# Kernel optimization log

Hardware: AMD Instinct MI355X
Metric: run time of the kernel (lower is better)

Reference implementation:

```python
import jax, jax.numpy as jnp
import numpy as np

CH = 256  # channels

def setup_inputs() -> dict:
    key = jax.random.key(0)
    ks = jax.random.split(key, 9)
    B, H, W = 8, 64, 64
    c8, c2 = CH // 8, CH // 2
    s = lambda fan_in: 1.0 / np.sqrt(fan_in)
    return {
        "x": jax.random.normal(ks[0], (B, H, W, CH), dtype=jnp.float32),
        "Wq": jax.random.normal(ks[1], (CH, c8), dtype=jnp.float32) * s(CH),
        "bq": jnp.zeros((c8,), dtype=jnp.float32),
        "Wk": jax.random.normal(ks[2], (CH, c8), dtype=jnp.float32) * s(CH),
        "bk": jnp.zeros((c8,), dtype=jnp.float32),
        "Wv": jax.random.normal(ks[3], (CH, c2), dtype=jnp.float32) * s(CH),
        "bv": jnp.zeros((c2,), dtype=jnp.float32),
        "Wo": jax.random.normal(ks[4], (c2, CH), dtype=jnp.float32) * s(c2),
        "bo": jnp.zeros((CH,), dtype=jnp.float32),
    }

def reference(x, Wq, bq, Wk, bk, Wv, bv, Wo, bo):
    B, H, W, C = x.shape
    # 1x1 convs are per-pixel matmuls over the channel dim
    q = x @ Wq + bq                      # [B,H,W,C/8]
    k = x @ Wk + bk                      # [B,H,W,C/8]
    v = x @ Wv + bv                      # [B,H,W,C/2]
    N = H * W
    qf = q.reshape(B, N, -1)
    kf = k.reshape(B, N, -1)
    vf = v.reshape(B, N, -1)
    # full self-attention over flattened spatial positions (no scaling, per source)
    scores = jnp.einsum('bnd,bmd->bnm', qf, kf)   # [B,N,N]
    attn = jax.nn.softmax(scores, axis=-1)
    out = jnp.einsum('bnm,bmd->bnd', attn, vf)    # [B,N,C/2]
    out = out.reshape(B, H, W, -1)
    return out @ Wo + bo + x
```

## Files before the change

### kernel.cpp

```cpp
#include <hip/hip_runtime.h>

typedef __attribute__((ext_vector_type(8))) short short8;
typedef __attribute__((ext_vector_type(8))) _Float16 half8;
typedef __attribute__((ext_vector_type(2))) float f32x2;
typedef __attribute__((ext_vector_type(4))) float f32x4;
typedef __attribute__((ext_vector_type(16))) float f32x16;

__device__ __forceinline__ unsigned short f2bf(float f) {
  unsigned int u = __float_as_uint(f);
  u += 0x7fffu + ((u >> 16) & 1u);
  return (unsigned short)(u >> 16);
}
__device__ __forceinline__ float bf2f(unsigned short h) {
  return __uint_as_float(((unsigned int)h) << 16);
}
__device__ __forceinline__ unsigned int cvtpk(float a, float b) {
  unsigned int r;
  asm("v_cvt_pk_bf16_f32 %0, %1, %2" : "=v"(r) : "v"(a), "v"(b));
  return r;
}
__device__ __forceinline__ unsigned short f2h(float f) {
  unsigned int r;
  asm("v_cvt_f16_f32 %0, %1" : "=v"(r) : "v"(f));
  return (unsigned short)r;
}
__device__ __forceinline__ float lo16f(unsigned int u) { return __uint_as_float(u << 16); }
__device__ __forceinline__ float hi16f(unsigned int u) { return __uint_as_float(u & 0xffff0000u); }
__device__ __forceinline__ short8 ld8(const unsigned short* p) {
  return *(const short8*)p;
}
__device__ __forceinline__ half8 ld8h(const unsigned short* p) {
  return *(const half8*)p;
}
__device__ __forceinline__ int swap23(int x) {
  return (x & 0x13) | ((x & 4) << 1) | ((x & 8) >> 1);
}
#define MFMA(a, b, c) __builtin_amdgcn_mfma_f32_16x16x32_bf16((a), (b), (c), 0, 0, 0)
#define MFMA32(a, b, c) __builtin_amdgcn_mfma_f32_32x32x16_bf16((a), (b), (c), 0, 0, 0)
#define MFMA32H(a, b, c) __builtin_amdgcn_mfma_f32_32x32x16_f16((a), (b), (c), 0, 0, 0)
#define LOG2E 1.4426950408889634f

typedef const __attribute__((address_space(1))) unsigned int* gas_u32p;
typedef __attribute__((address_space(3))) unsigned int* las_u32p;

__global__ void prep_weights(const float* __restrict__ Wq, const float* __restrict__ Wk,
                             const float* __restrict__ Wv, const float* __restrict__ Wo,
                             unsigned short* __restrict__ Wth, unsigned short* __restrict__ Wtl,
                             unsigned short* __restrict__ WoT) {
  int idx = blockIdx.x * 256 + threadIdx.x;
  if (idx < 192 * 256) {
    int o = idx >> 8, c = idx & 255;
    float w = (o < 32) ? Wq[c * 32 + o] : (o < 64) ? Wk[c * 32 + (o - 32)] : Wv[c * 128 + (o - 64)];
    unsigned short h = f2bf(w);
    Wth[idx] = h;
    Wtl[idx] = f2bf(w - bf2f(h));
  } else if (idx < 192 * 256 + 256 * 128) {
    int j = idx - 192 * 256;
    int c = j >> 7, d = j & 127;
    WoT[j] = f2bf(Wo[d * 256 + c]);
  }
}

__global__ __launch_bounds__(256) void proj_qkv(
    const float* __restrict__ x,
    const unsigned short* __restrict__ Wth, const unsigned short* __restrict__ Wtl,
    const float* __restrict__ bq, const float* __restrict__ bk, const float* __restrict__ bv,
    unsigned short* __restrict__ qh, unsigned short* __restrict__ KVF) {
  __shared__ unsigned short xsh[32][264];
  __shared__ unsigned short xsl[32][264];
  const int pix0 = blockIdx.x * 32;
  const int b = pix0 >> 12;
  const int nloc0 = pix0 & 4095;
  const int tid = threadIdx.x;

#pragma unroll
  for (int i = 0; i < 8; ++i) {
    int chunk = i * 256 + tid;
    int row = chunk >> 6;
    int c4 = (chunk & 63) * 4;
    float4 v = *(const float4*)(x + (size_t)(pix0 + row) * 256 + c4);
    unsigned int h01 = cvtpk(v.x, v.y), h23 = cvtpk(v.z, v.w);
    unsigned int l01 = cvtpk(v.x - lo16f(h01), v.y - hi16f(h01));
    unsigned int l23 = cvtpk(v.z - lo16f(h23), v.w - hi16f(h23));
    uint2 hp, lp;
    hp.x = h01; hp.y = h23;
    lp.x = l01; lp.y = l23;
    *(uint2*)&xsh[row][c4] = hp;
    *(uint2*)&xsl[row][c4] = lp;
  }
  __syncthreads();

  const int wave = tid >> 6, lane = tid & 63, l = lane & 15, qd = lane >> 4;
#pragma unroll
  for (int si = 0; si < 3; ++si) {
    const int sub = wave + si * 4;
    const int outc0 = sub * 16;
    if (si == 0) {
      const int outc = outc0 + l;
      const float bias = (outc < 32) ? bq[outc] : bk[outc - 32];
      f32x4 acc[2];
      acc[0] = (f32x4){bias, bias, bias, bias};
      acc[1] = (f32x4){bias, bias, bias, bias};
#pragma unroll
      for (int kc = 0; kc < 8; ++kc) {
        short8 whf = ld8(Wth + (size_t)(outc0 + l) * 256 + kc * 32 + qd * 8);
        short8 wlf = ld8(Wtl + (size_t)(outc0 + l) * 256 + kc * 32 + qd * 8);
#pragma unroll
        for (int m = 0; m < 2; ++m) {
          short8 xhf = ld8(&xsh[m * 16 + l][kc * 32 + qd * 8]);
          short8 xlf = ld8(&xsl[m * 16 + l][kc * 32 + qd * 8]);
          acc[m] = MFMA(xlf, whf, acc[m]);
          acc[m] = MFMA(xhf, wlf, acc[m]);
          acc[m] = MFMA(xhf, whf, acc[m]);
        }
      }
      if (outc < 32) {
#pragma unroll
        for (int m = 0; m < 2; ++m)
#pragma unroll
          for (int r = 0; r < 4; ++r) {
            const size_t pixel = (size_t)pix0 + m * 16 + 4 * qd + r;
            qh[pixel * 32 + outc] = f2h(acc[m][r] * LOG2E);
          }
      } else {
        const int kd = outc - 32;
        const int step = kd >> 4, hh = (kd >> 3) & 1, e = kd & 7;
#pragma unroll
        for (int m = 0; m < 2; ++m)
#pragma unroll
          for (int r = 0; r < 4; ++r) {
            const int nl = nloc0 + m * 16 + 4 * qd + r;
            const int nt = nl >> 6, j = nl & 63, kt = j >> 5;
            const int lpos = swap23(j & 31);
            const size_t koff = (size_t)(b * 64 + nt) * 10240 +
                                (kt * 2 + step) * 512 + (hh * 32 + lpos) * 8 + e;
            KVF[koff] = f2h(acc[m][r]);
          }
      }
    } else {
      const int dv0 = outc0 - 64;
      const float b0 = bv[dv0 + 4 * qd + 0], b1 = bv[dv0 + 4 * qd + 1];
      const float b2 = bv[dv0 + 4 * qd + 2], b3 = bv[dv0 + 4 * qd + 3];
      f32x4 acc[2];
      acc[0] = (f32x4){b0, b1, b2, b3};
      acc[1] = (f32x4){b0, b1, b2, b3};
#pragma unroll
      for (int kc = 0; kc < 8; ++kc) {
        short8 whf = ld8(Wth + (size_t)(outc0 + l) * 256 + kc * 32 + qd * 8);
#pragma unroll
        for (int m = 0; m < 2; ++m) {
          short8 xhf = ld8(&xsh[m * 16 + l][kc * 32 + qd * 8]);
          acc[m] = MFMA(whf, xhf, acc[m]);
        }
      }
#pragma unroll
      for (int m = 0; m < 2; ++m)
#pragma unroll
        for (int r = 0; r < 4; ++r) {
          const int dv = dv0 + 4 * qd + r;
          const int dt = dv >> 5, lam = dv & 31;
          const int nl = nloc0 + m * 16 + l;
          const int nt = nl >> 6, j = nl & 63;
          const int ks = j >> 4, hh = (j >> 3) & 1, e = j & 7;
          const size_t voff = (size_t)(b * 64 + nt) * 10240 + 2048 +
                              (dt * 4 + ks) * 512 + (hh * 32 + lam) * 8 + e;
          KVF[voff] = (unsigned short)cvtpk(acc[m][r], acc[m][r]);
        }
    }
  }
}

__device__ __forceinline__ void stage_kv(const unsigned short* __restrict__ src,
                                         unsigned short* dst, int wave, int lane) {
#pragma unroll
  for (int i = 0; i < 5; ++i) {
    const int c = wave * 5 + i;
    __builtin_amdgcn_global_load_lds(
        (gas_u32p)(const void*)(src + c * 512 + lane * 8),
        (las_u32p)(void*)(dst + c * 512), 16, 0, 0);
  }
}

__global__ __launch_bounds__(256, 2) void flash_attn(
    const unsigned short* __restrict__ qh,
    const unsigned short* __restrict__ KVF, unsigned short* __restrict__ opart,
    float* __restrict__ lstat) {
  __shared__ unsigned short kv[2][10240];
  const int b = blockIdx.x & 7;
  const int r7 = blockIdx.x >> 3;
  const int tile = r7 & 15;
  const int split = r7 >> 4;
  const int wave = threadIdx.x >> 6;
  const int lane = threadIdx.x & 63;
  const int lam = lane & 31;
  const int h = lane >> 5;
  const int m0 = tile * 256 + wave * 64;
  const int nt0 = split * 16;

  const unsigned short* qh_b = qh + (size_t)b * 4096 * 32;
  const unsigned short* kv_b = KVF + (size_t)b * 64 * 10240;

  half8 qf[2][2];
#pragma unroll
  for (int t = 0; t < 2; ++t)
#pragma unroll
    for (int step = 0; step < 2; ++step)
      qf[t][step] = ld8h(qh_b + (size_t)(m0 + t * 32 + lam) * 32 + step * 16 + h * 8);

  f32x16 acc0[4], acc1[4];
#pragma unroll
  for (int dt = 0; dt < 4; ++dt)
#pragma unroll
    for (int e = 0; e < 16; ++e) { acc0[dt][e] = 0.f; acc1[dt][e] = 0.f; }
  f32x2 lr0 = (f32x2){0.f, 0.f}, lr1 = (f32x2){0.f, 0.f};

  stage_kv(kv_b + (size_t)nt0 * 10240, &kv[0][0], wave, lane);
  __syncthreads();

  int cur = 0;
#pragma unroll 1
  for (int it = 0; it < 16; ++it) {
    if (it < 15)
      stage_kv(kv_b + (size_t)(nt0 + it + 1) * 10240, &kv[cur ^ 1][0], wave, lane);

    const unsigned short* cb = &kv[cur][0];

    half8 k0a = ld8h(cb + 0 * 512 + lane * 8);
    half8 k0b = ld8h(cb + 1 * 512 + lane * 8);
    f32x16 z0, z1;
#pragma unroll
    for (int e = 0; e < 16; ++e) { z0[e] = 0.f; z1[e] = 0.f; }
    __builtin_amdgcn_s_setprio(1);
    z0 = MFMA32H(k0a, qf[0][0], z0);
    z0 = MFMA32H(k0b, qf[0][1], z0);
    z1 = MFMA32H(k0a, qf[1][0], z1);
    z1 = MFMA32H(k0b, qf[1][1], z1);
    __builtin_amdgcn_s_setprio(0);
    unsigned int ppA0[8], ppA1[8];
#pragma unroll
    for (int g = 0; g < 8; ++g) {
      float a0 = __builtin_amdgcn_exp2f(z0[2 * g]);
      float a1 = __builtin_amdgcn_exp2f(z0[2 * g + 1]);
      lr0 += (f32x2){a0, a1};
      ppA0[g] = cvtpk(a0, a1);
      float c0 = __builtin_amdgcn_exp2f(z1[2 * g]);
      float c1 = __builtin_amdgcn_exp2f(z1[2 * g + 1]);
      lr1 += (f32x2){c0, c1};
      ppA1[g] = cvtpk(c0, c1);
    }

    half8 k1a = ld8h(cb + 2 * 512 + lane * 8);
    half8 k1b = ld8h(cb + 3 * 512 + lane * 8);
    f32x16 w0, w1;
#pragma unroll
    for (int e = 0; e < 16; ++e) { w0[e] = 0.f; w1[e] = 0.f; }
    __builtin_amdgcn_s_setprio(1);
    w0 = MFMA32H(k1a, qf[0][0], w0);
    w0 = MFMA32H(k1b, qf[0][1], w0);
    w1 = MFMA32H(k1a, qf[1][0], w1);
    w1 = MFMA32H(k1b, qf[1][1], w1);
#pragma unroll
    for (int kss = 0; kss < 2; ++kss) {
      union { unsigned int u[4]; short8 v; } pf0, pf1;
#pragma unroll
      for (int j = 0; j < 4; ++j) { pf0.u[j] = ppA0[4 * kss + j]; pf1.u[j] = ppA1[4 * kss + j]; }
#pragma unroll
      for (int dt = 0; dt < 4; ++dt) {
        short8 vfrag = *(const short8*)(cb + 2048 + (dt * 4 + kss) * 512 + lane * 8);
        acc0[dt] = MFMA32(vfrag, pf0.v, acc0[dt]);
        acc1[dt] = MFMA32(vfrag, pf1.v, acc1[dt]);
      }
    }
    __builtin_amdgcn_s_setprio(0);
    unsigned int ppB0[8], ppB1[8];
#pragma unroll
    for (int g = 0; g < 8; ++g) {
      float a0 = __builtin_amdgcn_exp2f(w0[2 * g]);
      float a1 = __builtin_amdgcn_exp2f(w0[2 * g + 1]);
      lr0 += (f32x2){a0, a1};
      ppB0[g] = cvtpk(a0, a1);
      float c0 = __builtin_amdgcn_exp2f(w1[2 * g]);
      float c1 = __builtin_amdgcn_exp2f(w1[2 * g + 1]);
      lr1 += (f32x2){c0, c1};
      ppB1[g] = cvtpk(c0, c1);
    }
    __builtin_amdgcn_s_setprio(1);
#pragma unroll
    for (int kss = 0; kss < 2; ++kss) {
      union { unsigned int u[4]; short8 v; } pf0, pf1;
#pragma unroll
      for (int j = 0; j < 4; ++j) { pf0.u[j] = ppB0[4 * kss + j]; pf1.u[j] = ppB1[4 * kss + j]; }
#pragma unroll
      for (int dt = 0; dt < 4; ++dt) {
        short8 vfrag = *(const short8*)(cb + 2048 + (dt * 4 + 2 + kss) * 512 + lane * 8);
        acc0[dt] = MFMA32(vfrag, pf0.v, acc0[dt]);
        acc1[dt] = MFMA32(vfrag, pf1.v, acc1[dt]);
      }
    }
    __builtin_amdgcn_s_setprio(0);

    __syncthreads();
    cur ^= 1;
  }

  {
    const float lrun = lr0.x + lr0.y;
    const float ltot = lrun + __shfl_xor(lrun, 32);
    const int grow = b * 4096 + m0 + lam;
    if (h == 0) lstat[split * 32768 + grow] = ltot;
    const size_t obase = ((size_t)split * 32768 + grow) * 128;
#pragma unroll
    for (int dt = 0; dt < 4; ++dt)
#pragma unroll
      for (int g = 0; g < 8; ++g) {
        int r = 2 * g;
        int dv = dt * 32 + (r & 3) + 8 * (r >> 2) + 4 * h;
        *(unsigned int*)(opart + obase + dv) = cvtpk(acc0[dt][r], acc0[dt][r + 1]);
      }
  }
  {
    const float lrun = lr1.x + lr1.y;
    const float ltot = lrun + __shfl_xor(lrun, 32);
    const int grow = b * 4096 + m0 + 32 + lam;
    if (h == 0) lstat[split * 32768 + grow] = ltot;
    const size_t obase = ((size_t)split * 32768 + grow) * 128;
#pragma unroll
    for (int dt = 0; dt < 4; ++dt)
#pragma unroll
      for (int g = 0; g < 8; ++g) {
        int r = 2 * g;
        int dv = dt * 32 + (r & 3) + 8 * (r >> 2) + 4 * h;
        *(unsigned int*)(opart + obase + dv) = cvtpk(acc1[dt][r], acc1[dt][r + 1]);
      }
  }
}

__global__ __launch_bounds__(256) void combine_splits(
    const unsigned short* __restrict__ opart, const float* __restrict__ lstat,
    unsigned short* __restrict__ ao) {
  const int tid = threadIdx.x;
  const int row = blockIdx.x * 16 + (tid >> 4);
  const int col = (tid & 15) * 8;
  float den = lstat[row] + lstat[32768 + row] + lstat[65536 + row] + lstat[98304 + row];
  float inv = 1.f / den;
  float o[8] = {0.f, 0.f, 0.f, 0.f, 0.f, 0.f, 0.f, 0.f};
#pragma unroll
  for (int s = 0; s < 4; ++s) {
    uint4 v = *(const uint4*)(opart + ((size_t)s * 32768 + row) * 128 + col);
    unsigned int uu[4] = {v.x, v.y, v.z, v.w};
#pragma unroll
    for (int j = 0; j < 4; ++j) {
      o[2 * j]     += bf2f((unsigned short)(uu[j] & 0xffff));
      o[2 * j + 1] += bf2f((unsigned short)(uu[j] >> 16));
    }
  }
  uint4 outv;
  outv.x = cvtpk(o[0] * inv, o[1] * inv);
  outv.y = cvtpk(o[2] * inv, o[3] * inv);
  outv.z = cvtpk(o[4] * inv, o[5] * inv);
  outv.w = cvtpk(o[6] * inv, o[7] * inv);
  *(uint4*)(ao + (size_t)row * 128 + col) = outv;
}

__global__ __launch_bounds__(256) void out_proj(
    const unsigned short* __restrict__ ao, const unsigned short* __restrict__ WoT,
    const float* __restrict__ bo, const float* __restrict__ x, float* __restrict__ out) {
  const int pix0 = blockIdx.x * 64;
  const int wave = threadIdx.x >> 6, lane = threadIdx.x & 63, l = lane & 15, qd = lane >> 4;
  const int base = pix0 + wave * 16;
  short8 af[4];
#pragma unroll
  for (int kc = 0; kc < 4; ++kc)
    af[kc] = ld8(ao + (size_t)(base + l) * 128 + kc * 32 + qd * 8);
#pragma unroll
  for (int sub = 0; sub < 16; ++sub) {
    const int c0 = sub * 16 + 4 * qd;
    float4 bb = *(const float4*)(bo + c0);
    f32x4 acc = (f32x4){bb.x, bb.y, bb.z, bb.w};
#pragma unroll
    for (int kc = 0; kc < 4; ++kc) {
      short8 wf = ld8(WoT + (size_t)(sub * 16 + l) * 128 + kc * 32 + qd * 8);
      acc = MFMA(wf, af[kc], acc);
    }
    float4 xv = *(const float4*)(x + (size_t)(base + l) * 256 + c0);
    float4 res;
    res.x = acc[0] + xv.x;
    res.y = acc[1] + xv.y;
    res.z = acc[2] + xv.z;
    res.w = acc[3] + xv.w;
    *(float4*)(out + (size_t)(base + l) * 256 + c0) = res;
  }
}

extern "C" void kernel_launch(void* const* d_in, const int* in_sizes, int n_in,
                              void* d_out, int out_size, void* d_ws, size_t ws_size,
                              hipStream_t stream) {
  const float* x  = (const float*)d_in[0];
  const float* Wq = (const float*)d_in[1];
  const float* bq = (const float*)d_in[2];
  const float* Wk = (const float*)d_in[3];
  const float* bk = (const float*)d_in[4];
  const float* Wv = (const float*)d_in[5];
  const float* bv = (const float*)d_in[6];
  const float* Wo = (const float*)d_in[7];
  const float* bo = (const float*)d_in[8];

  char* ws = (char*)d_ws;
  unsigned short* qh  = (unsigned short*)(ws + 0);
  unsigned short* KVF = (unsigned short*)(ws + 2097152);
  unsigned short* ao  = (unsigned short*)(ws + 12582912);
  unsigned short* Wth = (unsigned short*)(ws + 20971520);
  unsigned short* Wtl = (unsigned short*)(ws + 21069824);
  unsigned short* WoT = (unsigned short*)(ws + 21168128);
  float*          lst = (float*)(ws + 21233664);
  unsigned short* opart = (unsigned short*)d_out;

  prep_weights<<<320, 256, 0, stream>>>(Wq, Wk, Wv, Wo, Wth, Wtl, WoT);
  proj_qkv<<<1024, 256, 0, stream>>>(x, Wth, Wtl, bq, bk, bv, qh, KVF);
  flash_attn<<<512, 256, 0, stream>>>(qh, KVF, opart, lst);
  combine_splits<<<2048, 256, 0, stream>>>(opart, lst, ao);
  out_proj<<<512, 256, 0, stream>>>(ao, WoT, bo, x, (float*)d_out);
}
```

Measured before the change: 191.4 us.

## Halve rows per wave and use three KV splits with more blocks

The flash attention kernel now gives each wave 32 query rows instead of 64 and splits the key range into 3 uneven chunks instead of 4. This triples the block count relative to tiles and allows 3 blocks per CU via launch bounds. The combine kernel now sums 3 partials. The goal is to improve occupancy and load balance and to cut the combine traffic. The trade-off is less K/V reuse per LDS stage, so each query row needs twice the staging traffic.

```diff
diff --git a/kernel.cpp b/kernel.cpp
--- a/kernel.cpp
+++ b/kernel.cpp
@@ -181,120 +181,105 @@
   }
 }
 
-__global__ __launch_bounds__(256, 2) void flash_attn(
+__global__ __launch_bounds__(256, 3) void flash_attn(
     const unsigned short* __restrict__ qh,
     const unsigned short* __restrict__ KVF, unsigned short* __restrict__ opart,
     float* __restrict__ lstat) {
   __shared__ unsigned short kv[2][10240];
   const int b = blockIdx.x & 7;
   const int r7 = blockIdx.x >> 3;
-  const int tile = r7 & 15;
-  const int split = r7 >> 4;
+  const int tile = r7 & 31;
+  const int split = r7 >> 5;
   const int wave = threadIdx.x >> 6;
   const int lane = threadIdx.x & 63;
   const int lam = lane & 31;
   const int h = lane >> 5;
-  const int m0 = tile * 256 + wave * 64;
-  const int nt0 = split * 16;
+  const int m0 = tile * 128 + wave * 32;
+  const int nt_begin = (split * 64 + 2) / 3;
+  const int nt_end = ((split + 1) * 64 + 2) / 3;
 
   const unsigned short* qh_b = qh + (size_t)b * 4096 * 32;
   const unsigned short* kv_b = KVF + (size_t)b * 64 * 10240;
 
-  half8 qf[2][2];
-#pragma unroll
-  for (int t = 0; t < 2; ++t)
-#pragma unroll
-    for (int step = 0; step < 2; ++step)
-      qf[t][step] = ld8h(qh_b + (size_t)(m0 + t * 32 + lam) * 32 + step * 16 + h * 8);
-
-  f32x16 acc0[4], acc1[4];
+  half8 qf[2];
+#pragma unroll
+  for (int step = 0; step < 2; ++step)
+    qf[step] = ld8h(qh_b + (size_t)(m0 + lam) * 32 + step * 16 + h * 8);
+
+  f32x16 acc[4];
 #pragma unroll
   for (int dt = 0; dt < 4; ++dt)
 #pragma unroll
-    for (int e = 0; e < 16; ++e) { acc0[dt][e] = 0.f; acc1[dt][e] = 0.f; }
-  f32x2 lr0 = (f32x2){0.f, 0.f}, lr1 = (f32x2){0.f, 0.f};
-
-  stage_kv(kv_b + (size_t)nt0 * 10240, &kv[0][0], wave, lane);
+    for (int e = 0; e < 16; ++e) acc[dt][e] = 0.f;
+  f32x2 lr = (f32x2){0.f, 0.f};
+
+  stage_kv(kv_b + (size_t)nt_begin * 10240, &kv[0][0], wave, lane);
   __syncthreads();
 
   int cur = 0;
 #pragma unroll 1
-  for (int it = 0; it < 16; ++it) {
-    if (it < 15)
-      stage_kv(kv_b + (size_t)(nt0 + it + 1) * 10240, &kv[cur ^ 1][0], wave, lane);
+  for (int it = nt_begin; it < nt_end; ++it) {
+    if (it + 1 < nt_end)
+      stage_kv(kv_b + (size_t)(it + 1) * 10240, &kv[cur ^ 1][0], wave, lane);
 
     const unsigned short* cb = &kv[cur][0];
 
     half8 k0a = ld8h(cb + 0 * 512 + lane * 8);
     half8 k0b = ld8h(cb + 1 * 512 + lane * 8);
-    f32x16 z0, z1;
-#pragma unroll
-    for (int e = 0; e < 16; ++e) { z0[e] = 0.f; z1[e] = 0.f; }
+    f32x16 z;
+#pragma unroll
+    for (int e = 0; e < 16; ++e) z[e] = 0.f;
     __builtin_amdgcn_s_setprio(1);
-    z0 = MFMA32H(k0a, qf[0][0], z0);
-    z0 = MFMA32H(k0b, qf[0][1], z0);
-    z1 = MFMA32H(k0a, qf[1][0], z1);
-    z1 = MFMA32H(k0b, qf[1][1], z1);
+    z = MFMA32H(k0a, qf[0], z);
+    z = MFMA32H(k0b, qf[1], z);
     __builtin_amdgcn_s_setprio(0);
-    unsigned int ppA0[8], ppA1[8];
+    unsigned int ppA[8];
 #pragma unroll
     for (int g = 0; g < 8; ++g) {
-      float a0 = __builtin_amdgcn_exp2f(z0[2 * g]);
-      float a1 = __builtin_amdgcn_exp2f(z0[2 * g + 1]);
-      lr0 += (f32x2){a0, a1};
-      ppA0[g] = cvtpk(a0, a1);
-      float c0 = __builtin_amdgcn_exp2f(z1[2 * g]);
-      float c1 = __builtin_amdgcn_exp2f(z1[2 * g + 1]);
-      lr1 += (f32x2){c0, c1};
-      ppA1[g] = cvtpk(c0, c1);
+      float a0 = __builtin_amdgcn_exp2f(z[2 * g]);
+      float a1 = __builtin_amdgcn_exp2f(z[2 * g + 1]);
+      lr += (f32x2){a0, a1};
+      ppA[g] = cvtpk(a0, a1);
     }
 
     half8 k1a = ld8h(cb + 2 * 512 + lane * 8);
     half8 k1b = ld8h(cb + 3 * 512 + lane * 8);
-    f32x16 w0, w1;
-#pragma unroll
-    for (int e = 0; e < 16; ++e) { w0[e] = 0.f; w1[e] = 0.f; }
+    f32x16 w;
+#pragma unroll
+    for (int e = 0; e < 16; ++e) w[e] = 0.f;
     __builtin_amdgcn_s_setprio(1);
-    w0 = MFMA32H(k1a, qf[0][0], w0);
-    w0 = MFMA32H(k1b, qf[0][1], w0);
-    w1 = MFMA32H(k1a, qf[1][0], w1);
-    w1 = MFMA32H(k1b, qf[1][1], w1);
+    w = MFMA32H(k1a, qf[0], w);
+    w = MFMA32H(k1b, qf[1], w);
 #pragma unroll
     for (int kss = 0; kss < 2; ++kss) {
-      union { unsigned int u[4]; short8 v; } pf0, pf1;
-#pragma unroll
-      for (int j = 0; j < 4; ++j) { pf0.u[j] = ppA0[4 * kss + j]; pf1.u[j] = ppA1[4 * kss + j]; }
+      union { unsigned int u[4]; short8 v; } pf;
+#pragma unroll
+      for (int j = 0; j < 4; ++j) pf.u[j] = ppA[4 * kss + j];
 #pragma unroll
       for (int dt = 0; dt < 4; ++dt) {
         short8 vfrag = *(const short8*)(cb + 2048 + (dt * 4 + kss) * 512 + lane * 8);
-        acc0[dt] = MFMA32(vfrag, pf0.v, acc0[dt]);
-        acc1[dt] = MFMA32(vfrag, pf1.v, acc1[dt]);
+        acc[dt] = MFMA32(vfrag, pf.v, acc[dt]);
       }
     }
     __builtin_amdgcn_s_setprio(0);
-    unsigned int ppB0[8], ppB1[8];
+    unsigned int ppB[8];
 #pragma unroll
     for (int g = 0; g < 8; ++g) {
-      float a0 = __builtin_amdgcn_exp2f(w0[2 * g]);
-      float a1 = __builtin_amdgcn_exp2f(w0[2 * g + 1]);
-      lr0 += (f32x2){a0, a1};
-      ppB0[g] = cvtpk(a0, a1);
-      float c0 = __builtin_amdgcn_exp2f(w1[2 * g]);
-      float c1 = __builtin_amdgcn_exp2f(w1[2 * g + 1]);
-      lr1 += (f32x2){c0, c1};
-      ppB1[g] = cvtpk(c0, c1);
+      float a0 = __builtin_amdgcn_exp2f(w[2 * g]);
+      float a1 = __builtin_amdgcn_exp2f(w[2 * g + 1]);
+      lr += (f32x2){a0, a1};
+      ppB[g] = cvtpk(a0, a1);
     }
     __builtin_amdgcn_s_setprio(1);
 #pragma unroll
     for (int kss = 0; kss < 2; ++kss) {
-      union { unsigned int u[4]; short8 v; } pf0, pf1;
-#pragma unroll
-      for (int j = 0; j < 4; ++j) { pf0.u[j] = ppB0[4 * kss + j]; pf1.u[j] = ppB1[4 * kss + j]; }
+      union { unsigned int u[4]; short8 v; } pf;
+#pragma unroll
+      for (int j = 0; j < 4; ++j) pf.u[j] = ppB[4 * kss + j];
 #pragma unroll
       for (int dt = 0; dt < 4; ++dt) {
         short8 vfrag = *(const short8*)(cb + 2048 + (dt * 4 + 2 + kss) * 512 + lane * 8);
-        acc0[dt] = MFMA32(vfrag, pf0.v, acc0[dt]);
-        acc1[dt] = MFMA32(vfrag, pf1.v, acc1[dt]);
+        acc[dt] = MFMA32(vfrag, pf.v, acc[dt]);
       }
     }
     __builtin_amdgcn_s_setprio(0);
@@ -303,36 +288,19 @@
     cur ^= 1;
   }
 
-  {
-    const float lrun = lr0.x + lr0.y;
-    const float ltot = lrun + __shfl_xor(lrun, 32);
-    const int grow = b * 4096 + m0 + lam;
-    if (h == 0) lstat[split * 32768 + grow] = ltot;
-    const size_t obase = ((size_t)split * 32768 + grow) * 128;
-#pragma unroll
-    for (int dt = 0; dt < 4; ++dt)
-#pragma unroll
-      for (int g = 0; g < 8; ++g) {
-        int r = 2 * g;
-        int dv = dt * 32 + (r & 3) + 8 * (r >> 2) + 4 * h;
-        *(unsigned int*)(opart + obase + dv) = cvtpk(acc0[dt][r], acc0[dt][r + 1]);
-      }
-  }
-  {
-    const float lrun = lr1.x + lr1.y;
-    const float ltot = lrun + __shfl_xor(lrun, 32);
-    const int grow = b * 4096 + m0 + 32 + lam;
-    if (h == 0) lstat[split * 32768 + grow] = ltot;
-    const size_t obase = ((size_t)split * 32768 + grow) * 128;
-#pragma unroll
-    for (int dt = 0; dt < 4; ++dt)
-#pragma unroll
-      for (int g = 0; g < 8; ++g) {
-        int r = 2 * g;
-        int dv = dt * 32 + (r & 3) + 8 * (r >> 2) + 4 * h;
-        *(unsigned int*)(opart + obase + dv) = cvtpk(acc1[dt][r], acc1[dt][r + 1]);
-      }
-  }
+  const float lrun = lr.x + lr.y;
+  const float ltot = lrun + __shfl_xor(lrun, 32);
+  const int grow = b * 4096 + m0 + lam;
+  if (h == 0) lstat[split * 32768 + grow] = ltot;
+  const size_t obase = ((size_t)split * 32768 + grow) * 128;
+#pragma unroll
+  for (int dt = 0; dt < 4; ++dt)
+#pragma unroll
+    for (int g = 0; g < 8; ++g) {
+      int r = 2 * g;
+      int dv = dt * 32 + (r & 3) + 8 * (r >> 2) + 4 * h;
+      *(unsigned int*)(opart + obase + dv) = cvtpk(acc[dt][r], acc[dt][r + 1]);
+    }
 }
 
 __global__ __launch_bounds__(256) void combine_splits(
@@ -341,11 +309,11 @@
   const int tid = threadIdx.x;
   const int row = blockIdx.x * 16 + (tid >> 4);
   const int col = (tid & 15) * 8;
-  float den = lstat[row] + lstat[32768 + row] + lstat[65536 + row] + lstat[98304 + row];
+  float den = lstat[row] + lstat[32768 + row] + lstat[65536 + row];
   float inv = 1.f / den;
   float o[8] = {0.f, 0.f, 0.f, 0.f, 0.f, 0.f, 0.f, 0.f};
 #pragma unroll
-  for (int s = 0; s < 4; ++s) {
+  for (int s = 0; s < 3; ++s) {
     uint4 v = *(const uint4*)(opart + ((size_t)s * 32768 + row) * 128 + col);
     unsigned int uu[4] = {v.x, v.y, v.z, v.w};
 #pragma unroll
@@ -417,7 +385,7 @@
 
   prep_weights<<<320, 256, 0, stream>>>(Wq, Wk, Wv, Wo, Wth, Wtl, WoT);
   proj_qkv<<<1024, 256, 0, stream>>>(x, Wth, Wtl, bq, bk, bv, qh, KVF);
-  flash_attn<<<512, 256, 0, stream>>>(qh, KVF, opart, lst);
+  flash_attn<<<768, 256, 0, stream>>>(qh, KVF, opart, lst);
   combine_splits<<<2048, 256, 0, stream>>>(opart, lst, ao);
   out_proj<<<512, 256, 0, stream>>>(ao, WoT, bo, x, (float*)d_out);
 }
```

Measured after the change: 193.2 us. About the same (+0.9%).
